# Optimization experiments

Measured on AMD Instinct MI355X. Metric: run time of the kernel, lower is better.

Reference implementation:

```python
import jax, jax.numpy as jnp
import numpy as np

K_NEIGHBORS = 5  # n_neighbors
EPS = 1e-6


def setup_inputs() -> dict:
    key = jax.random.key(0)
    k1, k2, k3 = jax.random.split(key, 3)
    N, M, D, OUT = 4096, 16384, 32, 16
    x = jax.random.normal(k1, (N, D), dtype=jnp.float32)
    train_x = jax.random.normal(k2, (M, D), dtype=jnp.float32)
    train_y = jax.random.normal(k3, (M, OUT), dtype=jnp.float32)
    weights = jnp.zeros((D,), dtype=jnp.float32)  # nn.Parameter init
    return {"x": x, "train_x": train_x, "train_y": train_y, "weights": weights}


def reference(x, train_x, train_y, weights):
    # eval-mode forward of WeightedIDW (p=2, out_of_k unused in eval)
    scale = jnp.exp(weights)                      # [D]
    xq = x / scale                                # [N, D]
    xt = train_x / scale                          # [M, D]
    # p=2 distance: sum((x-y)^2) + eps, then sqrt — via Gram identity
    sq = (jnp.sum(xq * xq, axis=1, keepdims=True)
          + jnp.sum(xt * xt, axis=1)[None, :]
          - 2.0 * (xq @ xt.T))                    # [N, M]
    dist = jnp.sqrt(jnp.maximum(sq, 0.0) + EPS)   # [N, M]
    dinv = 1.0 / dist                             # inverse-distance weights
    # k-th largest inverse distance per row = min of top-k values
    top_vals = jax.lax.top_k(dinv, K_NEIGHBORS)[0]  # [N, K]
    min_val = top_vals[:, -1:]                      # [N, 1]
    w = jnp.where(dinv >= min_val, dinv, 0.0)       # keep only top-k (ties kept, as in torch)
    w = w / jnp.sum(w, axis=1, keepdims=True)       # row-normalize
    return w @ train_y                              # [N, OUT]
```

## Files before the change

kernel.cpp:

```cpp
#include <hip/hip_runtime.h>

#define N_Q 4096
#define M_T 16384
#define D_ 32
#define OUT_ 16
#define EPS_ 1e-6f
#define NCHUNK 16
#define CPTS (M_T / NCHUNK)
#define TPTS 256
#define NTILE (CPTS / TPTS)
#define NKEY 5
#define NCAND 12
#define BIAS_ 128.0f
#define KMASK 0xFFFFC000u

typedef short bf16x8 __attribute__((ext_vector_type(8)));
typedef float f32x4 __attribute__((ext_vector_type(4)));

static __device__ __forceinline__ unsigned short f2bf(float f) {
  unsigned int u = __float_as_uint(f);
  return (unsigned short)((u + 0x7FFFu + ((u >> 16) & 1u)) >> 16);
}
static __device__ __forceinline__ float bf2f(unsigned short h) {
  return __uint_as_float(((unsigned int)h) << 16);
}

__device__ __forceinline__ void chain5(unsigned int (&a)[NKEY], unsigned int v) {
#pragma unroll
  for (int i = 0; i < NKEY; ++i) {
    unsigned int lo = min(a[i], v);
    v = max(a[i], v);
    a[i] = lo;
  }
}
__device__ __forceinline__ void chain12(unsigned int (&a)[NCAND], unsigned int v) {
#pragma unroll
  for (int i = 0; i < NCAND; ++i) {
    unsigned int lo = min(a[i], v);
    v = max(a[i], v);
    a[i] = lo;
  }
}
__device__ __forceinline__ void insert5f(float (&s)[5], int (&id)[5], float v, int vi) {
  float cs = v; int ci = vi;
#pragma unroll
  for (int k = 0; k < 5; ++k) {
    bool lt = cs < s[k];
    float ts = s[k]; int ti = id[k];
    s[k] = lt ? cs : ts;  id[k] = lt ? ci : ti;
    cs   = lt ? ts : cs;  ci    = lt ? ti : ci;
  }
}

__global__ __launch_bounds__(256) void p0_prep(const float* __restrict__ x,
                                               const float* __restrict__ tx,
                                               const float* __restrict__ wts,
                                               float* __restrict__ xqs,
                                               float* __restrict__ xts,
                                               float* __restrict__ xqn,
                                               float* __restrict__ xtn,
                                               unsigned short* __restrict__ xq_h,
                                               unsigned short* __restrict__ xq_l,
                                               unsigned short* __restrict__ xt_h) {
  int gid = blockIdx.x * 256 + threadIdx.x;
  int row = gid >> 2;
  int g   = gid & 3;
  if (row >= N_Q + M_T) return;
  bool isq = row < N_Q;
  const float* src; float* dstf; unsigned short* dh; float* ndst; int ri;
  if (isq) { src = x;  dstf = xqs; dh = xq_h; ndst = xqn; ri = row; }
  else     { src = tx; dstf = xts; dh = xt_h; ndst = xtn; ri = row - N_Q; }
  float4 a = *(const float4*)(src + (size_t)ri * D_ + g * 8);
  float4 b = *(const float4*)(src + (size_t)ri * D_ + g * 8 + 4);
  float v[8] = {a.x, a.y, a.z, a.w, b.x, b.y, b.z, b.w};
  float nrm = 0.f;
  unsigned short hh[8], ll[8];
#pragma unroll
  for (int i = 0; i < 8; ++i) {
    float s = expf(wts[g * 8 + i]);
    v[i] /= s;
    nrm = fmaf(v[i], v[i], nrm);
    hh[i] = f2bf(v[i]);
    ll[i] = f2bf(v[i] - bf2f(hh[i]));
  }
  *(float4*)(dstf + (size_t)ri * D_ + g * 8)     = make_float4(v[0], v[1], v[2], v[3]);
  *(float4*)(dstf + (size_t)ri * D_ + g * 8 + 4) = make_float4(v[4], v[5], v[6], v[7]);
  nrm += __shfl_xor(nrm, 1);
  nrm += __shfl_xor(nrm, 2);
  if (g == 0) ndst[ri] = nrm;
  size_t ti = (size_t)(ri >> 4) * 512 + g * 128 + (ri & 15) * 8;
  uint4 hv;
  hv.x = hh[0] | (hh[1] << 16); hv.y = hh[2] | (hh[3] << 16);
  hv.z = hh[4] | (hh[5] << 16); hv.w = hh[6] | (hh[7] << 16);
  *(uint4*)(dh + ti) = hv;
  if (isq) {
    uint4 lv;
    lv.x = ll[0] | (ll[1] << 16); lv.y = ll[2] | (ll[3] << 16);
    lv.z = ll[4] | (ll[5] << 16); lv.w = ll[6] | (ll[7] << 16);
    *(uint4*)(xq_l + ti) = lv;
  }
}

__global__ __launch_bounds__(256, 1) void p1_topk(const unsigned short* __restrict__ xq_h,
                                                  const unsigned short* __restrict__ xq_l,
                                                  const unsigned short* __restrict__ xt_h,
                                                  const float* __restrict__ xtn,
                                                  unsigned int* __restrict__ pkey) {
  __shared__ __align__(16) unsigned short sh[TPTS * D_];
  __shared__ float stn[TPTS];
  const int t = threadIdx.x;
  const int w = t >> 6, lane = t & 63;
  const int p = lane & 15, g = lane >> 4;
  const int chunk = blockIdx.x;
  const int qb = blockIdx.y * 64 + w * 16;

  const size_t abase = (size_t)(qb >> 4) * 512 + g * 128 + p * 8;
  const bf16x8 ah = *(const bf16x8*)(xq_h + abase);
  const bf16x8 al = *(const bf16x8*)(xq_l + abase);
  const f32x4 zero = {0.f, 0.f, 0.f, 0.f};

  unsigned int key[4][NKEY];
#pragma unroll
  for (int r = 0; r < 4; ++r)
#pragma unroll
    for (int k = 0; k < NKEY; ++k) key[r][k] = 0xFFFFFFFFu;

  for (int tt = 0; tt < NTILE; ++tt) {
    const int pbase = chunk * CPTS + tt * TPTS;
    const size_t gb = (size_t)(pbase >> 4) * 512;
    __syncthreads();
#pragma unroll
    for (int c = 0; c < 4; ++c) {
      __builtin_amdgcn_global_load_lds(
          (const __attribute__((address_space(1))) void*)(xt_h + gb + (size_t)(w * 4 + c) * 512 + (size_t)lane * 8),
          (__attribute__((address_space(3))) void*)(sh + (w * 4 + c) * 512),
          16, 0, 0);
    }
    stn[t] = xtn[pbase + t] + BIAS_;
    __syncthreads();

#pragma unroll 2
    for (int s = 0; s < 16; ++s) {
      const bf16x8 bh = *(const bf16x8*)(sh + s * 512 + lane * 8);
      const float tnB = stn[s * 16 + p];
      f32x4 acc = __builtin_amdgcn_mfma_f32_16x16x32_bf16(al, bh, zero, 0, 0, 0);
      acc = __builtin_amdgcn_mfma_f32_16x16x32_bf16(ah, bh, acc, 0, 0, 0);
      const unsigned int kor = (unsigned int)(pbase + s * 16 + p);
#pragma unroll
      for (int r = 0; r < 4; ++r) {
        float v = fmaf(-2.0f, acc[r], tnB);
        chain5(key[r], (__float_as_uint(v) & KMASK) | kor);
      }
    }
  }

#pragma unroll
  for (int r = 0; r < 4; ++r) {
#pragma unroll
    for (int step = 1; step < 16; step <<= 1) {
      unsigned int ov[NKEY];
#pragma unroll
      for (int k = 0; k < NKEY; ++k)
        ov[k] = (unsigned int)__shfl_xor((int)key[r][k], step);
#pragma unroll
      for (int k = 0; k < NKEY; ++k) chain5(key[r], ov[k]);
    }
    if (p < 5) {
      unsigned int val = key[r][0];
      val = (p == 1) ? key[r][1] : val;
      val = (p == 2) ? key[r][2] : val;
      val = (p == 3) ? key[r][3] : val;
      val = (p == 4) ? key[r][4] : val;
      pkey[((size_t)chunk * N_Q + (qb + g * 4 + r)) * 5 + p] = val;
    }
  }
}

__global__ __launch_bounds__(256) void p2_merge(const unsigned int* __restrict__ pkey,
                                                const float* __restrict__ xqs,
                                                const float* __restrict__ xqn,
                                                const float* __restrict__ xts,
                                                const float* __restrict__ xtn,
                                                const float* __restrict__ ty,
                                                float* __restrict__ out) {
  const int q    = (blockIdx.x * blockDim.x + threadIdx.x) >> 6;
  const int lane = threadIdx.x & 63;
  if (q >= N_Q) return;

  unsigned int s[NCAND];
#pragma unroll
  for (int m = 0; m < NCAND; ++m) s[m] = 0xFFFFFFFFu;
  {
    int c = lane;
    int ch = c / 5, k = c - ch * 5;
    chain12(s, pkey[((size_t)ch * N_Q + q) * 5 + k]);
  }
  {
    unsigned int v = 0xFFFFFFFFu;
    if (lane < 16) {
      int c = 64 + lane;
      int ch = c / 5, k = c - ch * 5;
      v = pkey[((size_t)ch * N_Q + q) * 5 + k];
    }
    chain12(s, v);
  }

#pragma unroll
  for (int step = 1; step < 64; step <<= 1) {
    unsigned int ov[NCAND];
#pragma unroll
    for (int m = 0; m < NCAND; ++m) ov[m] = (unsigned int)__shfl_xor((int)s[m], step);
#pragma unroll
    for (int m = 0; m < NCAND; ++m) chain12(s, ov[m]);
  }

  unsigned int mykey = s[0];
#pragma unroll
  for (int m = 1; m < NCAND; ++m) mykey = (lane == m) ? s[m] : mykey;

  int   cidx = (int)(mykey & 0x3FFFu);
  float sqex = 3.0e38f;
  if (lane < NCAND) {
    float d = 0.f;
    const float* xr = xqs + (size_t)q * D_;
    const float* tr = xts + (size_t)cidx * D_;
#pragma unroll
    for (int c = 0; c < 8; ++c) {
      float4 a = *(const float4*)(xr + c * 4);
      float4 b = *(const float4*)(tr + c * 4);
      d = fmaf(a.x, b.x, d); d = fmaf(a.y, b.y, d);
      d = fmaf(a.z, b.z, d); d = fmaf(a.w, b.w, d);
    }
    sqex = fmaxf(xqn[q] + xtn[cidx] - 2.0f * d, 0.0f);
  }

  float s5[5]; int id5[5];
#pragma unroll
  for (int k = 0; k < 5; ++k) { s5[k] = 3.0e38f; id5[k] = 0; }
#pragma unroll
  for (int m = 0; m < NCAND; ++m) {
    float v  = __shfl(sqex, m);
    int   vi = __shfl(cidx, m);
    if (v < s5[4]) insert5f(s5, id5, v, vi);
  }

  float dinv[5]; float wsum = 0.f;
#pragma unroll
  for (int k = 0; k < 5; ++k) {
    dinv[k] = 1.0f / sqrtf(s5[k] + EPS_);
    wsum += dinv[k];
  }
  if (lane < OUT_) {
    float acc = 0.f;
#pragma unroll
    for (int k = 0; k < 5; ++k)
      acc = fmaf(dinv[k] / wsum, ty[(size_t)id5[k] * OUT_ + lane], acc);
    out[(size_t)q * OUT_ + lane] = acc;
  }
}

extern "C" void kernel_launch(void* const* d_in, const int* in_sizes, int n_in,
                              void* d_out, int out_size, void* d_ws, size_t ws_size,
                              hipStream_t stream) {
  const float* x   = (const float*)d_in[0];
  const float* tx  = (const float*)d_in[1];
  const float* ty  = (const float*)d_in[2];
  const float* wts = (const float*)d_in[3];
  float* out = (float*)d_out;

  char* ws = (char*)d_ws;
  size_t off = 0;
  float* xqs = (float*)(ws + off); off += (size_t)N_Q * D_ * 4;
  float* xts = (float*)(ws + off); off += (size_t)M_T * D_ * 4;
  float* xqn = (float*)(ws + off); off += (size_t)N_Q * 4;
  float* xtn = (float*)(ws + off); off += (size_t)M_T * 4;
  unsigned short* xq_h = (unsigned short*)(ws + off); off += (size_t)N_Q * D_ * 2;
  unsigned short* xq_l = (unsigned short*)(ws + off); off += (size_t)N_Q * D_ * 2;
  unsigned short* xt_h = (unsigned short*)(ws + off); off += (size_t)M_T * D_ * 2;
  unsigned int* pkey = (unsigned int*)(ws + off);

  p0_prep<<<dim3((N_Q + M_T) * 4 / 256), dim3(256), 0, stream>>>(
      x, tx, wts, xqs, xts, xqn, xtn, xq_h, xq_l, xt_h);
  p1_topk<<<dim3(NCHUNK, N_Q / 64), dim3(256), 0, stream>>>(
      xq_h, xq_l, xt_h, xtn, pkey);
  p2_merge<<<dim3(N_Q * 64 / 256), dim3(256), 0, stream>>>(
      pkey, xqs, xqn, xts, xtn, ty, out);
}
```

Baseline: 113.7 us.

## Double chunk split and merge per-block top-k through shared memory

Splits the training set into twice as many chunks, so p1 launches more blocks with half the tiles each. The cross-lane shuffle merge of per-lane top-5 lists is replaced by a two-stage merge through shared memory, which reuses the tile buffers via a union. p2 now merges 160 candidates per query instead of 80. This trades more parallelism in p1 for more partial-key traffic and a larger merge in p2.

```diff
diff --git a/kernel.cpp b/kernel.cpp
--- a/kernel.cpp
+++ b/kernel.cpp
@@ -5,7 +5,7 @@
 #define D_ 32
 #define OUT_ 16
 #define EPS_ 1e-6f
-#define NCHUNK 16
+#define NCHUNK 32
 #define CPTS (M_T / NCHUNK)
 #define TPTS 256
 #define NTILE (CPTS / TPTS)
@@ -101,18 +101,23 @@
   }
 }
 
+union P1Smem {
+  struct { unsigned short sh[TPTS * D_]; float stn[TPTS]; } loop;
+  struct { unsigned int kbuf[64 * 16 * NKEY]; unsigned int s1[64 * 4 * NKEY]; } mrg;
+};
+
 __global__ __launch_bounds__(256, 1) void p1_topk(const unsigned short* __restrict__ xq_h,
                                                   const unsigned short* __restrict__ xq_l,
                                                   const unsigned short* __restrict__ xt_h,
                                                   const float* __restrict__ xtn,
                                                   unsigned int* __restrict__ pkey) {
-  __shared__ __align__(16) unsigned short sh[TPTS * D_];
-  __shared__ float stn[TPTS];
+  __shared__ __align__(16) P1Smem sm;
   const int t = threadIdx.x;
   const int w = t >> 6, lane = t & 63;
   const int p = lane & 15, g = lane >> 4;
   const int chunk = blockIdx.x;
-  const int qb = blockIdx.y * 64 + w * 16;
+  const int qbB = blockIdx.y * 64;
+  const int qb  = qbB + w * 16;
 
   const size_t abase = (size_t)(qb >> 4) * 512 + g * 128 + p * 8;
   const bf16x8 ah = *(const bf16x8*)(xq_h + abase);
@@ -133,16 +138,16 @@
     for (int c = 0; c < 4; ++c) {
       __builtin_amdgcn_global_load_lds(
           (const __attribute__((address_space(1))) void*)(xt_h + gb + (size_t)(w * 4 + c) * 512 + (size_t)lane * 8),
-          (__attribute__((address_space(3))) void*)(sh + (w * 4 + c) * 512),
+          (__attribute__((address_space(3))) void*)(sm.loop.sh + (w * 4 + c) * 512),
           16, 0, 0);
     }
-    stn[t] = xtn[pbase + t] + BIAS_;
+    sm.loop.stn[t] = xtn[pbase + t] + BIAS_;
     __syncthreads();
 
 #pragma unroll 2
     for (int s = 0; s < 16; ++s) {
-      const bf16x8 bh = *(const bf16x8*)(sh + s * 512 + lane * 8);
-      const float tnB = stn[s * 16 + p];
+      const bf16x8 bh = *(const bf16x8*)(sm.loop.sh + s * 512 + lane * 8);
+      const float tnB = sm.loop.stn[s * 16 + p];
       f32x4 acc = __builtin_amdgcn_mfma_f32_16x16x32_bf16(al, bh, zero, 0, 0, 0);
       acc = __builtin_amdgcn_mfma_f32_16x16x32_bf16(ah, bh, acc, 0, 0, 0);
       const unsigned int kor = (unsigned int)(pbase + s * 16 + p);
@@ -154,25 +159,41 @@
     }
   }
 
+  __syncthreads();
 #pragma unroll
   for (int r = 0; r < 4; ++r) {
-#pragma unroll
-    for (int step = 1; step < 16; step <<= 1) {
-      unsigned int ov[NKEY];
-#pragma unroll
-      for (int k = 0; k < NKEY; ++k)
-        ov[k] = (unsigned int)__shfl_xor((int)key[r][k], step);
-#pragma unroll
-      for (int k = 0; k < NKEY; ++k) chain5(key[r], ov[k]);
-    }
-    if (p < 5) {
-      unsigned int val = key[r][0];
-      val = (p == 1) ? key[r][1] : val;
-      val = (p == 2) ? key[r][2] : val;
-      val = (p == 3) ? key[r][3] : val;
-      val = (p == 4) ? key[r][4] : val;
-      pkey[((size_t)chunk * N_Q + (qb + g * 4 + r)) * 5 + p] = val;
-    }
+    const int ql = w * 16 + g * 4 + r;
+#pragma unroll
+    for (int k = 0; k < NKEY; ++k)
+      sm.mrg.kbuf[(ql * 16 + p) * NKEY + k] = key[r][k];
+  }
+  __syncthreads();
+
+  {
+    const int ql = t & 63, quarter = t >> 6;
+    unsigned int m1[NKEY];
+#pragma unroll
+    for (int k = 0; k < NKEY; ++k) m1[k] = 0xFFFFFFFFu;
+    const unsigned int* src = sm.mrg.kbuf + (ql * 16 + quarter * 4) * NKEY;
+#pragma unroll
+    for (int i = 0; i < 4 * NKEY; ++i) chain5(m1, src[i]);
+    __syncthreads();
+#pragma unroll
+    for (int k = 0; k < NKEY; ++k)
+      sm.mrg.s1[(ql * 4 + quarter) * NKEY + k] = m1[k];
+  }
+  __syncthreads();
+
+  if (t < 64) {
+    unsigned int m2[NKEY];
+#pragma unroll
+    for (int k = 0; k < NKEY; ++k) m2[k] = 0xFFFFFFFFu;
+    const unsigned int* src = sm.mrg.s1 + t * 4 * NKEY;
+#pragma unroll
+    for (int i = 0; i < 4 * NKEY; ++i) chain5(m2, src[i]);
+#pragma unroll
+    for (int k = 0; k < NKEY; ++k)
+      pkey[((size_t)chunk * N_Q + (qbB + t)) * NKEY + k] = m2[k];
   }
 }
 
@@ -196,9 +217,14 @@
     chain12(s, pkey[((size_t)ch * N_Q + q) * 5 + k]);
   }
   {
+    int c = lane + 64;
+    int ch = c / 5, k = c - ch * 5;
+    chain12(s, pkey[((size_t)ch * N_Q + q) * 5 + k]);
+  }
+  {
     unsigned int v = 0xFFFFFFFFu;
-    if (lane < 16) {
-      int c = 64 + lane;
+    if (lane < 32) {
+      int c = 128 + lane;
       int ch = c / 5, k = c - ch * 5;
       v = pkey[((size_t)ch * N_Q + q) * 5 + k];
     }
```

After: 107.1 us. 1.06x faster.
